# Kernel optimization log

Measured on AMD Instinct MI355X. Metric: run time of the kernel, lower is better.

Reference implementation:

```python
import jax, jax.numpy as jnp
import numpy as np

B, S, D, H = 2, 2048, 2048, 16
NOPE, ROPE, V, C = 128, 64, 128, 512
EPS = 1e-6


def _rope(x, cos, sin):
    # x: [b,s,h,d] with d even; consecutive pairs form complex numbers (torch view_as_complex)
    b, s, h, d = x.shape
    x2 = x.reshape(b, s, h, d // 2, 2)
    xr, xi = x2[..., 0], x2[..., 1]
    c = cos[None, :, None, :]
    sn = sin[None, :, None, :]
    yr = xr * c - xi * sn
    yi = xr * sn + xi * c
    return jnp.stack([yr, yi], axis=-1).reshape(b, s, h, d)


def _rmsnorm(x, w):
    return x * jax.lax.rsqrt(jnp.mean(x * x, axis=-1, keepdims=True) + EPS) * w


def setup_inputs() -> dict:
    key = jax.random.key(0)
    ks = jax.random.split(key, 6)
    x = jax.random.normal(ks[0], (B, S, D), jnp.float32)
    # xavier-ish scaled weights (torch layout: [out, in])
    wq = jax.random.normal(ks[1], (H * (NOPE + ROPE), D), jnp.float32) * (D ** -0.5)
    wkv_a = jax.random.normal(ks[2], (C + ROPE, D), jnp.float32) * (D ** -0.5)
    kv_norm_w = jnp.ones((C,), jnp.float32)
    wkv_b = jax.random.normal(ks[3], (H * (NOPE + V), C), jnp.float32) * (C ** -0.5)
    wo = jax.random.normal(ks[4], (D, H * V), jnp.float32) * ((H * V) ** -0.5)
    # rope freqs (theta=10000), cos/sin of shape [S, ROPE//2]
    inv = 1.0 / (10000.0 ** (np.arange(0, ROPE, 2, dtype=np.float32) / ROPE))
    ang = np.outer(np.arange(S, dtype=np.float32), inv)
    cos = jnp.asarray(np.cos(ang), jnp.float32)
    sin = jnp.asarray(np.sin(ang), jnp.float32)
    # causal additive mask [S, S]
    idx = jnp.arange(S)
    mask = jnp.where(idx[None, :] <= idx[:, None], 0.0, -1e9).astype(jnp.float32)
    return dict(x=x, cos=cos, sin=sin, mask=mask, wq=wq, wkv_a=wkv_a,
                kv_norm_w=kv_norm_w, wkv_b=wkv_b, wo=wo)


def reference(x, cos, sin, mask, wq, wkv_a, kv_norm_w, wkv_b, wo):
    scale = (NOPE + ROPE) ** -0.5
    # Q projection -> [B,S,H,NOPE+ROPE]
    q = (x @ wq.T).reshape(B, S, H, NOPE + ROPE)
    q_nope, q_pe = q[..., :NOPE], q[..., NOPE:]
    q_pe = _rope(q_pe, cos, sin)
    # low-rank KV latent + shared rope key
    kvr = x @ wkv_a.T                      # [B,S,C+ROPE]
    kv, k_pe = kvr[..., :C], kvr[..., C:]
    k_pe = _rope(k_pe[:, :, None, :], cos, sin)[:, :, 0, :]   # [B,S,ROPE]
    # absorb-mode: fold wkv_b's nope part into q
    wb = wkv_b.reshape(H, NOPE + V, C)
    q_abs = jnp.einsum('bshd,hdc->bshc', q_nope, wb[:, :NOPE])
    kvn = _rmsnorm(kv, kv_norm_w)          # latent cache [B,S,C]
    scores = (jnp.einsum('bshc,btc->bsht', q_abs, kvn)
              + jnp.einsum('bshr,btr->bsht', q_pe, k_pe)) * scale
    scores = scores + mask[None, :, None, :]
    p = jax.nn.softmax(scores.astype(jnp.float32), axis=-1).astype(x.dtype)
    o = jnp.einsum('bsht,btc->bshc', p, kvn)
    o = jnp.einsum('bshc,hdc->bshd', o, wb[:, NOPE:])   # un-absorb value proj
    return o.reshape(B, S, H * V) @ wo.T
```

## Files before the change

kernel.cpp:

```cpp
#include <hip/hip_runtime.h>
#include <hip/hip_bf16.h>

#define B_ 2
#define S_ 2048
#define H_ 16

typedef unsigned short ushort_t;
typedef unsigned int uint_t;
typedef __attribute__((ext_vector_type(8))) short bf16x8;
typedef __attribute__((ext_vector_type(4))) float f32x4;

__device__ __forceinline__ ushort_t f2bf(float f) {
    uint_t u = __float_as_uint(f);
    return (ushort_t)((u + 0x7fffu + ((u >> 16) & 1u)) >> 16);
}
__device__ __forceinline__ float bf2f(ushort_t v) {
    return __uint_as_float(((uint_t)v) << 16);
}

__device__ __forceinline__ void gl_lds16(const ushort_t* g, ushort_t* l) {
    __builtin_amdgcn_global_load_lds(
        (const __attribute__((address_space(1))) unsigned int*)(unsigned long long)g,
        (__attribute__((address_space(3))) unsigned int*)(unsigned int)(unsigned long long)l,
        16, 0, 0);
}

__global__ __launch_bounds__(256) void cast_bf16(const float* __restrict__ src,
                                                 ushort_t* __restrict__ dst, int n)
{
    int i = (blockIdx.x * 256 + threadIdx.x) * 4;
    if (i < n) {
        float4 v = *(const float4*)(src + i);
        ushort_t pk[4] = { f2bf(v.x), f2bf(v.y), f2bf(v.z), f2bf(v.w) };
        *(uint2*)(dst + i) = *(const uint2*)pk;
    }
}

__global__ __launch_bounds__(256) void cast2_bf16(const float* __restrict__ src,
                                                  ushort_t* __restrict__ hi,
                                                  ushort_t* __restrict__ lo, int n)
{
    int i = (blockIdx.x * 256 + threadIdx.x) * 4;
    if (i < n) {
        float4 v = *(const float4*)(src + i);
        float vv[4] = { v.x, v.y, v.z, v.w };
        ushort_t ph[4], pl[4];
#pragma unroll
        for (int k = 0; k < 4; k++) {
            ph[k] = f2bf(vv[k]);
            pl[k] = f2bf(vv[k] - bf2f(ph[k]));
        }
        *(uint2*)(hi + i) = *(const uint2*)ph;
        *(uint2*)(lo + i) = *(const uint2*)pl;
    }
}

__global__ __launch_bounds__(256, 2) void gemm_bf16(const ushort_t* __restrict__ A,
                                                    const ushort_t* __restrict__ Bm,
                                                    float* __restrict__ Cf,
                                                    ushort_t* __restrict__ Cb,
                                                    int M, int N, int K,
                                                    int ldc, int Nreal, int mode)
{
    __shared__ __align__(16) ushort_t As[2][8192];
    __shared__ __align__(16) ushort_t Bs[2][8192];
    const int tid = threadIdx.x;
    const int wv = tid >> 6, lane = tid & 63, l16 = lane & 15, quad = lane >> 4;
    const int wm = wv >> 1, wn = wv & 1;
    const int m0 = blockIdx.y * 128, n0 = blockIdx.x * 128;
    const int srow = lane >> 3;
    const int sch  = ((lane & 7) ^ srow) * 8;

    f32x4 acc[16];
#pragma unroll
    for (int i = 0; i < 16; i++) acc[i] = (f32x4)(0.f);

#pragma unroll
    for (int p = 0; p < 4; p++) {
        int g = wv + p*4, row = g*8 + srow;
        int rowb = n0 + row; if (rowb > Nreal - 1) rowb = Nreal - 1;
        gl_lds16(A  + (size_t)(m0 + row) * K + sch, &As[0][g*512]);
        gl_lds16(Bm + (size_t)rowb * K + sch,       &Bs[0][g*512]);
    }
    __syncthreads();

    int cur = 0;
    for (int k0 = 0; k0 < K; k0 += 64) {
        if (k0 + 64 < K) {
#pragma unroll
            for (int p = 0; p < 4; p++) {
                int g = wv + p*4, row = g*8 + srow;
                int rowb = n0 + row; if (rowb > Nreal - 1) rowb = Nreal - 1;
                gl_lds16(A  + (size_t)(m0 + row) * K + k0 + 64 + sch, &As[cur^1][g*512]);
                gl_lds16(Bm + (size_t)rowb * K + k0 + 64 + sch,       &Bs[cur^1][g*512]);
            }
        }
#pragma unroll
        for (int ks = 0; ks < 2; ks++) {
            bf16x8 af[4], bfr[4];
#pragma unroll
            for (int mt = 0; mt < 4; mt++) {
                int row = wm*64 + mt*16 + l16;
                af[mt] = *(const bf16x8*)(&As[cur][row*64 + (((ks*4+quad) ^ (l16&7))*8)]);
            }
#pragma unroll
            for (int nt = 0; nt < 4; nt++) {
                int row = wn*64 + nt*16 + l16;
                bfr[nt] = *(const bf16x8*)(&Bs[cur][row*64 + (((ks*4+quad) ^ (l16&7))*8)]);
            }
#pragma unroll
            for (int mt = 0; mt < 4; mt++)
#pragma unroll
                for (int nt = 0; nt < 4; nt++)
                    acc[mt*4+nt] = __builtin_amdgcn_mfma_f32_16x16x32_bf16(af[mt], bfr[nt], acc[mt*4+nt], 0, 0, 0);
        }
        __syncthreads();
        cur ^= 1;
    }
#pragma unroll
    for (int mt = 0; mt < 4; mt++)
#pragma unroll
        for (int nt = 0; nt < 4; nt++) {
            int cc = n0 + wn*64 + nt*16 + l16;
            if (cc < Nreal) {
#pragma unroll
                for (int r = 0; r < 4; r++) {
                    size_t rr = m0 + wm*64 + mt*16 + quad*4 + r;
                    float v = acc[mt*4+nt][r];
                    if (mode == 1)      Cb[rr*ldc + cc] = f2bf(v);
                    else if (mode == 2) Cf[rr*ldc + cc] += v;
                    else                Cf[rr*ldc + cc] = v;
                }
            }
        }
}

__global__ __launch_bounds__(256, 2) void gemm_kv3(const ushort_t* __restrict__ Ahg,
                                                   const ushort_t* __restrict__ Alg,
                                                   const ushort_t* __restrict__ Bhg,
                                                   const ushort_t* __restrict__ Blg,
                                                   float* __restrict__ Cf)
{
    __shared__ __align__(16) ushort_t Ah[8192];
    __shared__ __align__(16) ushort_t Al[8192];
    __shared__ __align__(16) ushort_t Bh[8192];
    __shared__ __align__(16) ushort_t Bl[8192];
    const int tid = threadIdx.x;
    const int wv = tid >> 6, lane = tid & 63, l16 = lane & 15, quad = lane >> 4;
    const int wm = wv >> 1, wn = wv & 1;
    const int m0 = blockIdx.y * 128, n0 = blockIdx.x * 128;
    const int srow = lane >> 3;
    const int sch  = ((lane & 7) ^ srow) * 8;
    const int K = 2048;

    f32x4 acc[16];
#pragma unroll
    for (int i = 0; i < 16; i++) acc[i] = (f32x4)(0.f);

    for (int k0 = 0; k0 < K; k0 += 64) {
#pragma unroll
        for (int p = 0; p < 4; p++) {
            int g = wv + p*4, row = g*8 + srow;
            int rowb = n0 + row; if (rowb > 575) rowb = 575;
            gl_lds16(Ahg + (size_t)(m0 + row)*K + k0 + sch, Ah + g*512);
            gl_lds16(Alg + (size_t)(m0 + row)*K + k0 + sch, Al + g*512);
            gl_lds16(Bhg + (size_t)rowb*K + k0 + sch,       Bh + g*512);
            gl_lds16(Blg + (size_t)rowb*K + k0 + sch,       Bl + g*512);
        }
        __syncthreads();
#pragma unroll
        for (int ks = 0; ks < 2; ks++) {
            bf16x8 ah[4], al[4], bh[4], bl[4];
#pragma unroll
            for (int mt = 0; mt < 4; mt++) {
                int off = (wm*64 + mt*16 + l16)*64 + (((ks*4+quad) ^ (l16&7))*8);
                ah[mt] = *(const bf16x8*)(Ah + off);
                al[mt] = *(const bf16x8*)(Al + off);
            }
#pragma unroll
            for (int nt = 0; nt < 4; nt++) {
                int off = (wn*64 + nt*16 + l16)*64 + (((ks*4+quad) ^ (l16&7))*8);
                bh[nt] = *(const bf16x8*)(Bh + off);
                bl[nt] = *(const bf16x8*)(Bl + off);
            }
#pragma unroll
            for (int mt = 0; mt < 4; mt++)
#pragma unroll
                for (int nt = 0; nt < 4; nt++) {
                    acc[mt*4+nt] = __builtin_amdgcn_mfma_f32_16x16x32_bf16(ah[mt], bh[nt], acc[mt*4+nt], 0, 0, 0);
                    acc[mt*4+nt] = __builtin_amdgcn_mfma_f32_16x16x32_bf16(al[mt], bh[nt], acc[mt*4+nt], 0, 0, 0);
                    acc[mt*4+nt] = __builtin_amdgcn_mfma_f32_16x16x32_bf16(ah[mt], bl[nt], acc[mt*4+nt], 0, 0, 0);
                }
        }
        __syncthreads();
    }
#pragma unroll
    for (int mt = 0; mt < 4; mt++)
#pragma unroll
        for (int nt = 0; nt < 4; nt++) {
            int cc = n0 + wn*64 + nt*16 + l16;
            if (cc < 576) {
#pragma unroll
                for (int r = 0; r < 4; r++) {
                    size_t rr = m0 + wm*64 + mt*16 + quad*4 + r;
                    Cf[rr*576 + cc] = acc[mt*4+nt][r];
                }
            }
        }
}

__global__ __launch_bounds__(256, 2) void gemm_vp(const ushort_t* __restrict__ kvnb,
                                                  const ushort_t* __restrict__ wbvB,
                                                  ushort_t* __restrict__ vpT)
{
    __shared__ __align__(16) ushort_t As[2][8192];
    __shared__ __align__(16) ushort_t Bs[2][8192];
    const int tid = threadIdx.x;
    const int wv = tid >> 6, lane = tid & 63, l16 = lane & 15, quad = lane >> 4;
    const int wm = wv >> 1, wn = wv & 1;
    const int m0 = blockIdx.x * 128;
    const int h  = blockIdx.y;
    const ushort_t* Bh = wbvB + h*65536;
    const int srow = lane >> 3;
    const int sch  = ((lane & 7) ^ srow) * 8;

    f32x4 acc[16];
#pragma unroll
    for (int i = 0; i < 16; i++) acc[i] = (f32x4)(0.f);

#pragma unroll
    for (int p = 0; p < 4; p++) {
        int g = wv + p*4, row = g*8 + srow;
        gl_lds16(kvnb + (size_t)(m0 + row)*512 + sch, &As[0][g*512]);
        gl_lds16(Bh   + (size_t)row*512 + sch,        &Bs[0][g*512]);
    }
    __syncthreads();

    int cur = 0;
    for (int k0 = 0; k0 < 512; k0 += 64) {
        if (k0 + 64 < 512) {
#pragma unroll
            for (int p = 0; p < 4; p++) {
                int g = wv + p*4, row = g*8 + srow;
                gl_lds16(kvnb + (size_t)(m0 + row)*512 + k0 + 64 + sch, &As[cur^1][g*512]);
                gl_lds16(Bh   + (size_t)row*512 + k0 + 64 + sch,        &Bs[cur^1][g*512]);
            }
        }
#pragma unroll
        for (int ks = 0; ks < 2; ks++) {
            bf16x8 af[4], bfr[4];
#pragma unroll
            for (int mt = 0; mt < 4; mt++) {
                int row = wm*64 + mt*16 + l16;
                af[mt] = *(const bf16x8*)(&As[cur][row*64 + (((ks*4+quad) ^ (l16&7))*8)]);
            }
#pragma unroll
            for (int nt = 0; nt < 4; nt++) {
                int row = wn*64 + nt*16 + l16;
                bfr[nt] = *(const bf16x8*)(&Bs[cur][row*64 + (((ks*4+quad) ^ (l16&7))*8)]);
            }
#pragma unroll
            for (int mt = 0; mt < 4; mt++)
#pragma unroll
                for (int nt = 0; nt < 4; nt++)
                    acc[mt*4+nt] = __builtin_amdgcn_mfma_f32_16x16x32_bf16(af[mt], bfr[nt], acc[mt*4+nt], 0, 0, 0);
        }
        __syncthreads();
        cur ^= 1;
    }
#pragma unroll
    for (int mt = 0; mt < 4; mt++)
#pragma unroll
        for (int nt = 0; nt < 4; nt++) {
            int rr = m0 + wm*64 + mt*16 + quad*4;
            int bb = rr >> 11, t = rr & 2047;
            int cc = wn*64 + nt*16 + l16;
            ushort_t pk[4];
#pragma unroll
            for (int r = 0; r < 4; r++) pk[r] = f2bf(acc[mt*4+nt][r]);
            *(uint2*)(vpT + ((size_t)((bb*16 + h)*128 + cc))*2048 + t) = *(const uint2*)pk;
        }
}

__global__ __launch_bounds__(256) void prep_wb(const float* __restrict__ wkv_b,
                                               ushort_t* __restrict__ wbkT,
                                               ushort_t* __restrict__ wbvB)
{
    int u = blockIdx.x * 256 + threadIdx.x;
    {
        int h = u >> 16, rem = u & 65535, c = rem >> 7, d = rem & 127;
        wbkT[u] = f2bf(wkv_b[h*131072 + d*512 + c]);
    }
    {
        int h = u >> 16, rem = u & 65535;
        wbvB[u] = f2bf(wkv_b[h*131072 + 65536 + rem]);
    }
}

__global__ __launch_bounds__(256) void kv_norm_rope(const float* __restrict__ kvr,
                                                    const float* __restrict__ w,
                                                    const float* __restrict__ cosT,
                                                    const float* __restrict__ sinT,
                                                    ushort_t* __restrict__ kvnb,
                                                    ushort_t* __restrict__ kpeb)
{
    const int bs   = blockIdx.x * 4 + (threadIdx.x >> 6);
    const int lane = threadIdx.x & 63;
    const int s    = bs & (S_ - 1);
    const float* row = kvr + bs * 576;

    float4 v0 = *(const float4*)(row + lane*8);
    float4 v1 = *(const float4*)(row + lane*8 + 4);
    float ss = v0.x*v0.x + v0.y*v0.y + v0.z*v0.z + v0.w*v0.w
             + v1.x*v1.x + v1.y*v1.y + v1.z*v1.z + v1.w*v1.w;
#pragma unroll
    for (int off = 32; off >= 1; off >>= 1) ss += __shfl_xor(ss, off);
    const float rs = rsqrtf(ss * (1.0f/512.0f) + 1e-6f);

    float4 w0 = *(const float4*)(w + lane*8);
    float4 w1 = *(const float4*)(w + lane*8 + 4);
    float o[8];
    o[0] = v0.x*rs*w0.x; o[1] = v0.y*rs*w0.y; o[2] = v0.z*rs*w0.z; o[3] = v0.w*rs*w0.w;
    o[4] = v1.x*rs*w1.x; o[5] = v1.y*rs*w1.y; o[6] = v1.z*rs*w1.z; o[7] = v1.w*rs*w1.w;

    ushort_t pk[8];
#pragma unroll
    for (int p = 0; p < 8; p++) pk[p] = f2bf(o[p]);
    *(uint4*)(kvnb + (size_t)bs*512 + lane*8) = *(const uint4*)pk;

    if (lane < 32) {
        float xr = row[512 + 2*lane], xi = row[512 + 2*lane + 1];
        float c  = cosT[s*32 + lane], sn = sinT[s*32 + lane];
        ushort_t p2[2] = { f2bf(xr*c - xi*sn), f2bf(xr*sn + xi*c) };
        *(uint_t*)(kpeb + (size_t)bs*64 + 2*lane) = *(const uint_t*)p2;
    }
}

__device__ __forceinline__ void stage_tile(const ushort_t* kvn_b, const ushort_t* kpe_b,
                                           const ushort_t* vpT_h, ushort_t* ldsb,
                                           int t0, int buf, int w, int l16, int q8e)
{
    ushort_t* Fb = ldsb + buf*18432;
    ushort_t* Vb = ldsb + 36864 + buf*4096;
#pragma unroll
    for (int ii = 0; ii < 5; ii++) {
        int i = w + ii*8;
        if (i < 36) {
            int g2 = (i >= 18) ? 1 : 0;
            int ks = i - g2*18;
            int row = t0 + g2*16 + l16;
            const ushort_t* src = (ks < 16)
                ? (kvn_b + (size_t)row*512 + ks*32 + q8e)
                : (kpe_b + (size_t)row*64 + (ks-16)*32 + q8e);
            gl_lds16(src, Fb + i*512);
        }
    }
    {
        const ushort_t* src = vpT_h + (size_t)(w*16 + l16)*2048 + t0 + q8e;
        gl_lds16(src, Vb + w*512);
    }
}

__global__ __launch_bounds__(512, 2) void attn_mfma(
    const ushort_t* __restrict__ qb,
    const ushort_t* __restrict__ kvnb,
    const ushort_t* __restrict__ kpeb,
    const ushort_t* __restrict__ vpT,
    const float* __restrict__ cosT,
    const float* __restrict__ sinT,
    const ushort_t* __restrict__ wbkT,
    ushort_t* __restrict__ ovb)
{
    const int flat = blockIdx.x + 16*blockIdx.y + 256*blockIdx.z;
    const int b    = flat & 1;
    const int rem  = flat >> 1;
    const int h    = rem & 15;
    const int q0   = (15 - (rem >> 4)) << 7;

    const int tid  = threadIdx.x;
    const int w    = tid >> 6;
    const int lane = tid & 63;
    const int l16  = lane & 15;
    const int quad = lane >> 4;
    const int tl   = quad * 4;
    const int lb   = lane & 48;
    const int q8e  = quad * 8;
    const float scale = 0.07216878364870323f;

    __shared__ __align__(16) ushort_t lds[50176];

    const ushort_t* kvn_b = kvnb + (size_t)b*S_*512;
    const ushort_t* kpe_b = kpeb + (size_t)b*S_*64;
    const ushort_t* vpT_h = vpT + (size_t)(b*16 + h)*128*2048;

    const int r0    = q0 + w*16;
    const int rglob = r0 + l16;

    stage_tile(kvn_b, kpe_b, vpT_h, lds, 0, 0, w, l16, q8e);

    ushort_t* paw = lds + 18432 + w*2176;
    const ushort_t* qrow = qb + (size_t)(b*S_ + rglob)*3072 + h*192;
    bf16x8 qa[4], qf[18];
#pragma unroll
    for (int ks = 0; ks < 4; ks++)
        qa[ks] = *(const bf16x8*)(qrow + ks*32 + q8e);

    const ushort_t* wbk_h = wbkT + h*65536;
#pragma unroll
    for (int qq = 0; qq < 4; qq++) {
        f32x4 ab[8];
#pragma unroll
        for (int n = 0; n < 8; n++) ab[n] = (f32x4)(0.f);
#pragma unroll
        for (int n = 0; n < 8; n++) {
            const ushort_t* wp = wbk_h + (qq*128 + n*16 + l16)*128 + q8e;
#pragma unroll
            for (int ks = 0; ks < 4; ks++) {
                bf16x8 bw = *(const bf16x8*)(wp + ks*32);
                ab[n] = __builtin_amdgcn_mfma_f32_16x16x32_bf16(qa[ks], bw, ab[n], 0, 0, 0);
            }
        }
        asm volatile("" ::: "memory");
#pragma unroll
        for (int n = 0; n < 8; n++)
#pragma unroll
            for (int r = 0; r < 4; r++)
                paw[(tl + r)*136 + n*16 + l16] = f2bf(ab[n][r] * scale);
        asm volatile("" ::: "memory");
#pragma unroll
        for (int ks2 = 0; ks2 < 4; ks2++)
            qf[qq*4 + ks2] = *(const bf16x8*)(paw + l16*136 + ks2*32 + q8e);
        asm volatile("" ::: "memory");
    }

#pragma unroll
    for (int kk = 0; kk < 2; kk++) {
        int off = kk*32 + q8e;
        uint4 pv4 = *(const uint4*)(qrow + 128 + off);
        const ushort_t* pe = (const ushort_t*)&pv4;
        ushort_t pk[8];
#pragma unroll
        for (int u2 = 0; u2 < 4; u2++) {
            float xr = bf2f(pe[2*u2]), xi = bf2f(pe[2*u2+1]);
            int pi = (off >> 1) + u2;
            float c = cosT[rglob*32 + pi], sn = sinT[rglob*32 + pi];
            pk[2*u2]   = f2bf((xr*c  - xi*sn) * scale);
            pk[2*u2+1] = f2bf((xr*sn + xi*c ) * scale);
        }
        qf[16 + kk] = *(const bf16x8*)pk;
    }
    __syncthreads();

    f32x4 o[8];
#pragma unroll
    for (int n = 0; n < 8; n++) o[n] = (f32x4)(0.f);
    float m_s = -1e30f, l_s = 0.f;

    const int bniter = (q0 >> 5) + 4;
    const int wniter = ((r0 + 15) >> 5) + 1;
    ushort_t* ptw = lds + 45056 + w*640;
    int cur = 0;

#pragma unroll 1
    for (int it = 0; it < bniter; it++) {
        if (it + 1 < bniter)
            stage_tile(kvn_b, kpe_b, vpT_h, lds, (it+1)*32, cur ^ 1, w, l16, q8e);

        if (it < wniter) {
            const int t0 = it * 32;
            const ushort_t* Fb = lds + cur*18432;
            const ushort_t* Vb = lds + 36864 + cur*4096;

            __builtin_amdgcn_s_setprio(1);
            f32x4 s0 = (f32x4)(0.f), s1 = (f32x4)(0.f);
#pragma unroll
            for (int ks = 0; ks < 18; ks++) {
                bf16x8 kf0 = *(const bf16x8*)(Fb + ks*512 + lane*8);
                s0 = __builtin_amdgcn_mfma_f32_16x16x32_bf16(kf0, qf[ks], s0, 0, 0, 0);
                bf16x8 kf1 = *(const bf16x8*)(Fb + 9216 + ks*512 + lane*8);
                s1 = __builtin_amdgcn_mfma_f32_16x16x32_bf16(kf1, qf[ks], s1, 0, 0, 0);
            }
            __builtin_amdgcn_s_setprio(0);

            float pv[8];
            float mx = -1e30f;
#pragma unroll
            for (int reg = 0; reg < 4; reg++) {
                pv[reg]   = ((t0 + tl + reg)      <= rglob) ? s0[reg] : -1e30f;
                pv[4+reg] = ((t0 + 16 + tl + reg) <= rglob) ? s1[reg] : -1e30f;
                mx = fmaxf(mx, fmaxf(pv[reg], pv[4+reg]));
            }
            mx = fmaxf(mx, __shfl_xor(mx, 16));
            mx = fmaxf(mx, __shfl_xor(mx, 32));
            if (!__all(mx <= m_s)) {
                float mn = fmaxf(m_s, mx);
                float al = __expf(m_s - mn);
                m_s = mn;
                l_s *= al;
                f32x4 alv;
#pragma unroll
                for (int reg = 0; reg < 4; reg++) alv[reg] = __shfl(al, lb + tl + reg, 64);
#pragma unroll
                for (int n = 0; n < 8; n++) o[n] *= alv;
            }
            float ps = 0.f;
#pragma unroll
            for (int reg = 0; reg < 8; reg++) {
                pv[reg] = (pv[reg] > -1e29f) ? __expf(pv[reg] - m_s) : 0.f;
                ps += pv[reg];
            }
            ps += __shfl_xor(ps, 16);
            ps += __shfl_xor(ps, 32);
            l_s += ps;

            ushort_t pk4[8];
#pragma unroll
            for (int reg = 0; reg < 8; reg++) pk4[reg] = f2bf(pv[reg]);
            *(uint2*)(ptw + l16*40 + tl)      = *(const uint2*)(pk4);
            *(uint2*)(ptw + l16*40 + 16 + tl) = *(const uint2*)(pk4 + 4);
            asm volatile("" ::: "memory");
            bf16x8 ap = *(const bf16x8*)(ptw + l16*40 + q8e);
            asm volatile("" ::: "memory");

            __builtin_amdgcn_s_setprio(1);
#pragma unroll
            for (int n = 0; n < 8; n++) {
                bf16x8 bv = *(const bf16x8*)(Vb + n*512 + lane*8);
                o[n] = __builtin_amdgcn_mfma_f32_16x16x32_bf16(ap, bv, o[n], 0, 0, 0);
            }
            __builtin_amdgcn_s_setprio(0);
        }
        __syncthreads();
        cur ^= 1;
    }

    float linv = 1.f / l_s;
    f32x4 rlv;
#pragma unroll
    for (int reg = 0; reg < 4; reg++) rlv[reg] = __shfl(linv, lb + tl + reg, 64);

    ushort_t* orow = ovb + (size_t)(b*S_ + r0)*2048 + h*128;
#pragma unroll
    for (int n = 0; n < 8; n++)
#pragma unroll
        for (int reg = 0; reg < 4; reg++)
            orow[(size_t)(tl + reg)*2048 + n*16 + l16] = f2bf(o[n][reg] * rlv[reg]);
}

extern "C" void kernel_launch(void* const* d_in, const int* in_sizes, int n_in,
                              void* d_out, int out_size, void* d_ws, size_t ws_size,
                              hipStream_t stream) {
    const float* x     = (const float*)d_in[0];
    const float* cosT  = (const float*)d_in[1];
    const float* sinT  = (const float*)d_in[2];
    const float* wq    = (const float*)d_in[4];
    const float* wkv_a = (const float*)d_in[5];
    const float* kvw   = (const float*)d_in[6];
    const float* wkv_b = (const float*)d_in[7];
    const float* wo    = (const float*)d_in[8];
    float* out = (float*)d_out;

    ushort_t* qb   = (ushort_t*)d_ws;
    ushort_t* xb   = qb   + 12582912;
    ushort_t* wqb  = xb   + 8388608;
    ushort_t* wob  = wqb  + 6291456;
    ushort_t* ovb  = wob  + 4194304;
    ushort_t* kvnb = ovb  + 8388608;
    ushort_t* kpeb = kvnb + 2097152;
    ushort_t* kvnT = kpeb + 262144;
    ushort_t* wbkT = kvnT + 2097152;
    ushort_t* wbvB = wbkT + 1048576;
    float*    kvr  = (float*)(wbvB + 1048576);

    ushort_t* xlo  = ovb;
    ushort_t* wahi = wqb;
    ushort_t* walo = wqb + 1179648;
    ushort_t* vpT  = xb;

    dim3 blk(256);
    cast2_bf16<<<dim3(8192), blk, 0, stream>>>(x, xb, xlo, 8388608);
    cast_bf16<<<dim3(6144), blk, 0, stream>>>(wq, wqb, 6291456);
    cast_bf16<<<dim3(4096), blk, 0, stream>>>(wo, wob, 4194304);
    prep_wb<<<dim3(4096), blk, 0, stream>>>(wkv_b, wbkT, wbvB);
    gemm_bf16<<<dim3(24, 32), blk, 0, stream>>>(xb, wqb, nullptr, qb, 4096, 3072, 2048, 3072, 3072, 1);
    cast2_bf16<<<dim3(1152), blk, 0, stream>>>(wkv_a, wahi, walo, 1179648);
    gemm_kv3<<<dim3(5, 32), blk, 0, stream>>>(xb, xlo, wahi, walo, kvr);
    kv_norm_rope<<<dim3(1024), blk, 0, stream>>>(kvr, kvw, cosT, sinT, kvnb, kpeb);
    gemm_vp<<<dim3(32, 16), blk, 0, stream>>>(kvnb, wbvB, vpT);
    attn_mfma<<<dim3(16, 16, 2), dim3(512), 0, stream>>>(qb, kvnb, kpeb, vpT, cosT, sinT, wbkT, ovb);
    gemm_bf16<<<dim3(16, 32), blk, 0, stream>>>(ovb, wob, out, nullptr, 4096, 2048, 2048, 2048, 2048, 0);
}
```

Baseline: 533.1 us.

## Un-absorb key projection: precompute per-head keys instead of absorbing into queries

Adds a GEMM that multiplies the normalized latent cache by the nope part of wkv_b, producing per-head 128-dim keys, with the softmax scale folded into those keys and into k_pe. Attention then contracts over 192 dims instead of the 576-dim absorbed latent. This shrinks the per-tile LDS staging and the QK MFMA work, and removes the in-kernel query absorption. The cost is an extra key tensor per batch and head written to and read from memory. The wo cast is moved later so its buffer can be reused for the key tensor.

```diff
diff --git a/kernel.cpp b/kernel.cpp
--- a/kernel.cpp
+++ b/kernel.cpp
@@ -282,19 +282,88 @@
         }
 }
 
+__global__ __launch_bounds__(256, 2) void gemm_kp(const ushort_t* __restrict__ kvnb,
+                                                  const ushort_t* __restrict__ wbkN,
+                                                  ushort_t* __restrict__ kpb)
+{
+    __shared__ __align__(16) ushort_t As[2][8192];
+    __shared__ __align__(16) ushort_t Bs[2][8192];
+    const int tid = threadIdx.x;
+    const int wv = tid >> 6, lane = tid & 63, l16 = lane & 15, quad = lane >> 4;
+    const int wm = wv >> 1, wn = wv & 1;
+    const int m0 = blockIdx.x * 128;
+    const int h  = blockIdx.y;
+    const ushort_t* Bh = wbkN + h*65536;
+    const int srow = lane >> 3;
+    const int sch  = ((lane & 7) ^ srow) * 8;
+    const float scale = 0.07216878364870323f;
+
+    f32x4 acc[16];
+#pragma unroll
+    for (int i = 0; i < 16; i++) acc[i] = (f32x4)(0.f);
+
+#pragma unroll
+    for (int p = 0; p < 4; p++) {
+        int g = wv + p*4, row = g*8 + srow;
+        gl_lds16(kvnb + (size_t)(m0 + row)*512 + sch, &As[0][g*512]);
+        gl_lds16(Bh   + (size_t)row*512 + sch,        &Bs[0][g*512]);
+    }
+    __syncthreads();
+
+    int cur = 0;
+    for (int k0 = 0; k0 < 512; k0 += 64) {
+        if (k0 + 64 < 512) {
+#pragma unroll
+            for (int p = 0; p < 4; p++) {
+                int g = wv + p*4, row = g*8 + srow;
+                gl_lds16(kvnb + (size_t)(m0 + row)*512 + k0 + 64 + sch, &As[cur^1][g*512]);
+                gl_lds16(Bh   + (size_t)row*512 + k0 + 64 + sch,        &Bs[cur^1][g*512]);
+            }
+        }
+#pragma unroll
+        for (int ks = 0; ks < 2; ks++) {
+            bf16x8 af[4], bfr[4];
+#pragma unroll
+            for (int mt = 0; mt < 4; mt++) {
+                int row = wm*64 + mt*16 + l16;
+                af[mt] = *(const bf16x8*)(&As[cur][row*64 + (((ks*4+quad) ^ (l16&7))*8)]);
+            }
+#pragma unroll
+            for (int nt = 0; nt < 4; nt++) {
+                int row = wn*64 + nt*16 + l16;
+                bfr[nt] = *(const bf16x8*)(&Bs[cur][row*64 + (((ks*4+quad) ^ (l16&7))*8)]);
+            }
+#pragma unroll
+            for (int mt = 0; mt < 4; mt++)
+#pragma unroll
+                for (int nt = 0; nt < 4; nt++)
+                    acc[mt*4+nt] = __builtin_amdgcn_mfma_f32_16x16x32_bf16(af[mt], bfr[nt], acc[mt*4+nt], 0, 0, 0);
+        }
+        __syncthreads();
+        cur ^= 1;
+    }
+#pragma unroll
+    for (int mt = 0; mt < 4; mt++)
+#pragma unroll
+        for (int nt = 0; nt < 4; nt++) {
+            int cc = wn*64 + nt*16 + l16;
+#pragma unroll
+            for (int r = 0; r < 4; r++) {
+                int rr = m0 + wm*64 + mt*16 + quad*4 + r;
+                int bb = rr >> 11, t = rr & 2047;
+                kpb[((size_t)((bb*16 + h)*2048 + t))*128 + cc] = f2bf(acc[mt*4+nt][r] * scale);
+            }
+        }
+}
+
 __global__ __launch_bounds__(256) void prep_wb(const float* __restrict__ wkv_b,
-                                               ushort_t* __restrict__ wbkT,
+                                               ushort_t* __restrict__ wbkN,
                                                ushort_t* __restrict__ wbvB)
 {
     int u = blockIdx.x * 256 + threadIdx.x;
-    {
-        int h = u >> 16, rem = u & 65535, c = rem >> 7, d = rem & 127;
-        wbkT[u] = f2bf(wkv_b[h*131072 + d*512 + c]);
-    }
-    {
-        int h = u >> 16, rem = u & 65535;
-        wbvB[u] = f2bf(wkv_b[h*131072 + 65536 + rem]);
-    }
+    int h = u >> 16, rem = u & 65535;
+    wbkN[u] = f2bf(wkv_b[h*131072 + rem]);
+    wbvB[u] = f2bf(wkv_b[h*131072 + 65536 + rem]);
 }
 
 __global__ __launch_bounds__(256) void kv_norm_rope(const float* __restrict__ kvr,
@@ -308,6 +377,7 @@
     const int lane = threadIdx.x & 63;
     const int s    = bs & (S_ - 1);
     const float* row = kvr + bs * 576;
+    const float scale = 0.07216878364870323f;
 
     float4 v0 = *(const float4*)(row + lane*8);
     float4 v1 = *(const float4*)(row + lane*8 + 4);
@@ -331,44 +401,43 @@
     if (lane < 32) {
         float xr = row[512 + 2*lane], xi = row[512 + 2*lane + 1];
         float c  = cosT[s*32 + lane], sn = sinT[s*32 + lane];
-        ushort_t p2[2] = { f2bf(xr*c - xi*sn), f2bf(xr*sn + xi*c) };
+        ushort_t p2[2] = { f2bf((xr*c - xi*sn)*scale), f2bf((xr*sn + xi*c)*scale) };
         *(uint_t*)(kpeb + (size_t)bs*64 + 2*lane) = *(const uint_t*)p2;
     }
 }
 
-__device__ __forceinline__ void stage_tile(const ushort_t* kvn_b, const ushort_t* kpe_b,
+__device__ __forceinline__ void stage_tile(const ushort_t* kp_h, const ushort_t* kpe_b,
                                            const ushort_t* vpT_h, ushort_t* ldsb,
                                            int t0, int buf, int w, int l16, int q8e)
 {
-    ushort_t* Fb = ldsb + buf*18432;
-    ushort_t* Vb = ldsb + 36864 + buf*4096;
-#pragma unroll
-    for (int ii = 0; ii < 5; ii++) {
+    ushort_t* Fb = ldsb + buf*6144;
+    ushort_t* Vb = ldsb + 12288 + buf*4096;
+#pragma unroll
+    for (int ii = 0; ii < 3; ii++) {
         int i = w + ii*8;
-        if (i < 36) {
-            int g2 = (i >= 18) ? 1 : 0;
-            int ks = i - g2*18;
+        if (i < 12) {
+            int g2 = (i >= 6) ? 1 : 0;
+            int ks = i - g2*6;
             int row = t0 + g2*16 + l16;
-            const ushort_t* src = (ks < 16)
-                ? (kvn_b + (size_t)row*512 + ks*32 + q8e)
-                : (kpe_b + (size_t)row*64 + (ks-16)*32 + q8e);
+            const ushort_t* src = (ks < 4)
+                ? (kp_h + (size_t)row*128 + ks*32 + q8e)
+                : (kpe_b + (size_t)row*64 + (ks-4)*32 + q8e);
             gl_lds16(src, Fb + i*512);
-        }
-    }
-    {
-        const ushort_t* src = vpT_h + (size_t)(w*16 + l16)*2048 + t0 + q8e;
-        gl_lds16(src, Vb + w*512);
+        } else if (i < 20) {
+            int gv = i - 12;
+            const ushort_t* src = vpT_h + (size_t)(gv*16 + l16)*2048 + t0 + q8e;
+            gl_lds16(src, Vb + gv*512);
+        }
     }
 }
 
 __global__ __launch_bounds__(512, 2) void attn_mfma(
     const ushort_t* __restrict__ qb,
-    const ushort_t* __restrict__ kvnb,
+    const ushort_t* __restrict__ kpb,
     const ushort_t* __restrict__ kpeb,
     const ushort_t* __restrict__ vpT,
     const float* __restrict__ cosT,
     const float* __restrict__ sinT,
-    const ushort_t* __restrict__ wbkT,
     ushort_t* __restrict__ ovb)
 {
     const int flat = blockIdx.x + 16*blockIdx.y + 256*blockIdx.z;
@@ -385,54 +454,23 @@
     const int tl   = quad * 4;
     const int lb   = lane & 48;
     const int q8e  = quad * 8;
-    const float scale = 0.07216878364870323f;
-
-    __shared__ __align__(16) ushort_t lds[50176];
-
-    const ushort_t* kvn_b = kvnb + (size_t)b*S_*512;
+
+    __shared__ __align__(16) ushort_t lds[25600];
+
+    const ushort_t* kp_h  = kpb + (size_t)(b*16 + h)*2048*128;
     const ushort_t* kpe_b = kpeb + (size_t)b*S_*64;
     const ushort_t* vpT_h = vpT + (size_t)(b*16 + h)*128*2048;
 
     const int r0    = q0 + w*16;
     const int rglob = r0 + l16;
 
-    stage_tile(kvn_b, kpe_b, vpT_h, lds, 0, 0, w, l16, q8e);
-
-    ushort_t* paw = lds + 18432 + w*2176;
+    stage_tile(kp_h, kpe_b, vpT_h, lds, 0, 0, w, l16, q8e);
+
     const ushort_t* qrow = qb + (size_t)(b*S_ + rglob)*3072 + h*192;
-    bf16x8 qa[4], qf[18];
+    bf16x8 qf[6];
 #pragma unroll
     for (int ks = 0; ks < 4; ks++)
-        qa[ks] = *(const bf16x8*)(qrow + ks*32 + q8e);
-
-    const ushort_t* wbk_h = wbkT + h*65536;
-#pragma unroll
-    for (int qq = 0; qq < 4; qq++) {
-        f32x4 ab[8];
-#pragma unroll
-        for (int n = 0; n < 8; n++) ab[n] = (f32x4)(0.f);
-#pragma unroll
-        for (int n = 0; n < 8; n++) {
-            const ushort_t* wp = wbk_h + (qq*128 + n*16 + l16)*128 + q8e;
-#pragma unroll
-            for (int ks = 0; ks < 4; ks++) {
-                bf16x8 bw = *(const bf16x8*)(wp + ks*32);
-                ab[n] = __builtin_amdgcn_mfma_f32_16x16x32_bf16(qa[ks], bw, ab[n], 0, 0, 0);
-            }
-        }
-        asm volatile("" ::: "memory");
-#pragma unroll
-        for (int n = 0; n < 8; n++)
-#pragma unroll
-            for (int r = 0; r < 4; r++)
-                paw[(tl + r)*136 + n*16 + l16] = f2bf(ab[n][r] * scale);
-        asm volatile("" ::: "memory");
-#pragma unroll
-        for (int ks2 = 0; ks2 < 4; ks2++)
-            qf[qq*4 + ks2] = *(const bf16x8*)(paw + l16*136 + ks2*32 + q8e);
-        asm volatile("" ::: "memory");
-    }
-
+        qf[ks] = *(const bf16x8*)(qrow + ks*32 + q8e);
 #pragma unroll
     for (int kk = 0; kk < 2; kk++) {
         int off = kk*32 + q8e;
@@ -444,10 +482,10 @@
             float xr = bf2f(pe[2*u2]), xi = bf2f(pe[2*u2+1]);
             int pi = (off >> 1) + u2;
             float c = cosT[rglob*32 + pi], sn = sinT[rglob*32 + pi];
-            pk[2*u2]   = f2bf((xr*c  - xi*sn) * scale);
-            pk[2*u2+1] = f2bf((xr*sn + xi*c ) * scale);
-        }
-        qf[16 + kk] = *(const bf16x8*)pk;
+            pk[2*u2]   = f2bf(xr*c  - xi*sn);
+            pk[2*u2+1] = f2bf(xr*sn + xi*c );
+        }
+        qf[4 + kk] = *(const bf16x8*)pk;
     }
     __syncthreads();
 
@@ -458,26 +496,26 @@
 
     const int bniter = (q0 >> 5) + 4;
     const int wniter = ((r0 + 15) >> 5) + 1;
-    ushort_t* ptw = lds + 45056 + w*640;
+    ushort_t* ptw = lds + 20480 + w*640;
     int cur = 0;
 
 #pragma unroll 1
     for (int it = 0; it < bniter; it++) {
         if (it + 1 < bniter)
-            stage_tile(kvn_b, kpe_b, vpT_h, lds, (it+1)*32, cur ^ 1, w, l16, q8e);
+            stage_tile(kp_h, kpe_b, vpT_h, lds, (it+1)*32, cur ^ 1, w, l16, q8e);
 
         if (it < wniter) {
             const int t0 = it * 32;
-            const ushort_t* Fb = lds + cur*18432;
-            const ushort_t* Vb = lds + 36864 + cur*4096;
+            const ushort_t* Fb = lds + cur*6144;
+            const ushort_t* Vb = lds + 12288 + cur*4096;
 
             __builtin_amdgcn_s_setprio(1);
             f32x4 s0 = (f32x4)(0.f), s1 = (f32x4)(0.f);
 #pragma unroll
-            for (int ks = 0; ks < 18; ks++) {
+            for (int ks = 0; ks < 6; ks++) {
                 bf16x8 kf0 = *(const bf16x8*)(Fb + ks*512 + lane*8);
                 s0 = __builtin_amdgcn_mfma_f32_16x16x32_bf16(kf0, qf[ks], s0, 0, 0, 0);
-                bf16x8 kf1 = *(const bf16x8*)(Fb + 9216 + ks*512 + lane*8);
+                bf16x8 kf1 = *(const bf16x8*)(Fb + 3072 + ks*512 + lane*8);
                 s1 = __builtin_amdgcn_mfma_f32_16x16x32_bf16(kf1, qf[ks], s1, 0, 0, 0);
             }
             __builtin_amdgcn_s_setprio(0);
@@ -568,25 +606,27 @@
     ushort_t* kvnb = ovb  + 8388608;
     ushort_t* kpeb = kvnb + 2097152;
     ushort_t* kvnT = kpeb + 262144;
-    ushort_t* wbkT = kvnT + 2097152;
-    ushort_t* wbvB = wbkT + 1048576;
+    ushort_t* wbkN = kvnT + 2097152;
+    ushort_t* wbvB = wbkN + 1048576;
     float*    kvr  = (float*)(wbvB + 1048576);
 
     ushort_t* xlo  = ovb;
     ushort_t* wahi = wqb;
     ushort_t* walo = wqb + 1179648;
     ushort_t* vpT  = xb;
+    ushort_t* kpb  = wqb;
 
     dim3 blk(256);
     cast2_bf16<<<dim3(8192), blk, 0, stream>>>(x, xb, xlo, 8388608);
     cast_bf16<<<dim3(6144), blk, 0, stream>>>(wq, wqb, 6291456);
-    cast_bf16<<<dim3(4096), blk, 0, stream>>>(wo, wob, 4194304);
-    prep_wb<<<dim3(4096), blk, 0, stream>>>(wkv_b, wbkT, wbvB);
+    prep_wb<<<dim3(4096), blk, 0, stream>>>(wkv_b, wbkN, wbvB);
     gemm_bf16<<<dim3(24, 32), blk, 0, stream>>>(xb, wqb, nullptr, qb, 4096, 3072, 2048, 3072, 3072, 1);
     cast2_bf16<<<dim3(1152), blk, 0, stream>>>(wkv_a, wahi, walo, 1179648);
     gemm_kv3<<<dim3(5, 32), blk, 0, stream>>>(xb, xlo, wahi, walo, kvr);
     kv_norm_rope<<<dim3(1024), blk, 0, stream>>>(kvr, kvw, cosT, sinT, kvnb, kpeb);
     gemm_vp<<<dim3(32, 16), blk, 0, stream>>>(kvnb, wbvB, vpT);
-    attn_mfma<<<dim3(16, 16, 2), dim3(512), 0, stream>>>(qb, kvnb, kpeb, vpT, cosT, sinT, wbkT, ovb);
+    gemm_kp<<<dim3(32, 16), blk, 0, stream>>>(kvnb, wbkN, kpb);
+    attn_mfma<<<dim3(16, 16, 2), dim3(512), 0, stream>>>(qb, kpb, kpeb, vpT, cosT, sinT, ovb);
+    cast_bf16<<<dim3(4096), blk, 0, stream>>>(wo, wob, 4194304);
     gemm_bf16<<<dim3(16, 32), blk, 0, stream>>>(ovb, wob, out, nullptr, 4096, 2048, 2048, 2048, 2048, 0);
 }
```

After: 478.9 us. -10.2%, faster.
